# Kernel tuning notes

Hardware: AMD Instinct MI355X
Metric: run time of the kernel (lower is better)

Reference implementation:

```python
import jax, jax.numpy as jnp
import numpy as np

EPS = 1e-5

def layer_norm(x, w, b):
    # normalize over last two dims [N, H]
    mean = jnp.mean(x, axis=(-2, -1), keepdims=True)
    var = jnp.var(x, axis=(-2, -1), keepdims=True)
    return (x - mean) * jax.lax.rsqrt(var + EPS) * w + b

def lg_conv(x, edge_index, num_nodes):
    # LightGCN conv: symmetric-normalized neighbor sum (no self loops)
    src, dst = edge_index[0], edge_index[1]
    deg = jnp.zeros((num_nodes,), x.dtype).at[dst].add(1.0)
    dinv = jnp.where(deg > 0, jax.lax.rsqrt(jnp.maximum(deg, 1.0)), 0.0)
    norm = dinv[src] * dinv[dst]                      # [E]
    msgs = x[:, :, src, :] * norm[None, None, :, None]  # [B,P,E,H]
    return jnp.zeros_like(x).at[:, :, dst, :].add(msgs)

def setup_inputs() -> dict:
    key = jax.random.key(0)
    ks = jax.random.split(key, 4)
    B, P, N, H = 16, 12, 2048, 64
    E = 16384
    x = jax.random.normal(ks[0], (B, P, N, H), dtype=jnp.float32)
    edge_index = jax.random.randint(ks[1], (2, E), 0, N, dtype=jnp.int64)
    g_norm_w = jnp.ones((N, H), jnp.float32)
    g_norm_b = jnp.zeros((N, H), jnp.float32)
    t_norm_w = jnp.ones((N, H), jnp.float32)
    t_norm_b = jnp.zeros((N, H), jnp.float32)
    bound = 1.0 / np.sqrt(P)  # Conv2d default init range
    conv_w = jax.random.uniform(ks[2], (P, P), jnp.float32, -bound, bound)
    conv_b = jax.random.uniform(ks[3], (P,), jnp.float32, -bound, bound)
    return {"x": x, "edge_index": edge_index,
            "g_norm_w": g_norm_w, "g_norm_b": g_norm_b,
            "t_norm_w": t_norm_w, "t_norm_b": t_norm_b,
            "conv_w": conv_w, "conv_b": conv_b}

def reference(x, edge_index, g_norm_w, g_norm_b, t_norm_w, t_norm_b, conv_w, conv_b):
    N = x.shape[2]
    h = layer_norm(x, g_norm_w, g_norm_b)
    h = lg_conv(h, edge_index, N)
    h = layer_norm(h, t_norm_w, t_norm_b)
    # 1x1 Conv2d over channels = periods: [B,P,N,H] -> [B,Q,N,H]
    out = jnp.einsum('qp,bpnh->bqnh', conv_w, h) + conv_b[None, :, None, None]
    return out
```

## Files before the change

kernel.cpp:

```cpp
#include <hip/hip_runtime.h>

#define B_ 16
#define P_ 12
#define N_ 2048
#define H_ 64
#define E_ 16384
#define NH_ (N_*H_)
#define NG_ (B_*P_)

__global__ __launch_bounds__(256) void k_stats_x(const float* __restrict__ x,
                                                 float* __restrict__ partials ) {
    int g   = blockIdx.x >> 3;
    int seg = blockIdx.x & 7;
    const float4* xg = (const float4*)(x + (size_t)g * NH_);
    float s = 0.f, q = 0.f;
    int base = seg * 4096;
    #pragma unroll
    for (int i = 0; i < 16; ++i) {
        float4 v = xg[base + i*256 + threadIdx.x];
        s += v.x + v.y + v.z + v.w;
        q += v.x*v.x + v.y*v.y + v.z*v.z + v.w*v.w;
    }
    __shared__ float ls[4], lq[4];
    for (int off = 32; off; off >>= 1) { s += __shfl_down(s, off); q += __shfl_down(q, off); }
    int wid = threadIdx.x >> 6, lane = threadIdx.x & 63;
    if (!lane) { ls[wid] = s; lq[wid] = q; }
    __syncthreads();
    if (!threadIdx.x) {
        partials[blockIdx.x*2]   = ls[0]+ls[1]+ls[2]+ls[3];
        partials[blockIdx.x*2+1] = lq[0]+lq[1]+lq[2]+lq[3];
    }
}

__global__ __launch_bounds__(64) void k_finalize(const float* __restrict__ partials, int cnt,
                                                 float* __restrict__ mean, float* __restrict__ rstd) {
    int g = blockIdx.x, lane = threadIdx.x;
    float s = (lane < cnt) ? partials[(g*cnt+lane)*2]   : 0.f;
    float q = (lane < cnt) ? partials[(g*cnt+lane)*2+1] : 0.f;
    for (int off = 32; off; off >>= 1) { s += __shfl_down(s, off); q += __shfl_down(q, off); }
    if (!lane) {
        float m = s * (1.0f/NH_);
        float v = q * (1.0f/NH_) - m*m;
        mean[g] = m;
        rstd[g] = rsqrtf(v + 1e-5f);
    }
}

__global__ __launch_bounds__(1024) void k_build_csr(const int* __restrict__ ew,
                                                    int* __restrict__ rowPtr,
                                                    int* __restrict__ csrSrc,
                                                    float* __restrict__ csrW) {
    __shared__ int   sDeg[N_];
    __shared__ int   sA[N_];
    __shared__ int   sB[N_];
    __shared__ float sDinv[N_];
    __shared__ int   sFlag;
    int tid = threadIdx.x;
    if (!tid) sFlag = 1;
    for (int i = tid; i < N_; i += 1024) sDeg[i] = 0;
    __syncthreads();
    if (tid < 256) { if (ew[2*tid+1] != 0) atomicAnd(&sFlag, 0); }
    __syncthreads();
    int is64 = sFlag;
    for (int e = tid; e < E_; e += 1024) {
        int dst = is64 ? ew[2*(E_+e)] : ew[E_+e];
        atomicAdd(&sDeg[dst], 1);
    }
    __syncthreads();
    for (int i = tid; i < N_; i += 1024) {
        int d = sDeg[i];
        sDinv[i] = d > 0 ? rsqrtf((float)d) : 0.f;
        sA[i] = d;
    }
    __syncthreads();
    int* in = sA; int* out = sB;
    for (int st = 1; st < N_; st <<= 1) {
        for (int i = tid; i < N_; i += 1024) {
            int v = in[i];
            if (i >= st) v += in[i-st];
            out[i] = v;
        }
        __syncthreads();
        int* t = in; in = out; out = t;
    }
    for (int i = tid; i < N_; i += 1024) {
        int excl = in[i] - sDeg[i];
        rowPtr[i] = excl;
        out[i] = excl;
    }
    if (!tid) rowPtr[N_] = E_;
    __syncthreads();
    for (int e = tid; e < E_; e += 1024) {
        int src = is64 ? ew[2*e]       : ew[e];
        int dst = is64 ? ew[2*(E_+e)]  : ew[E_+e];
        int pos = atomicAdd(&out[dst], 1);
        csrSrc[pos] = src;
        csrW[pos] = sDinv[src] * sDinv[dst];
    }
}

__global__ __launch_bounds__(256) void k_gather(const float* __restrict__ x,
                                                const float* __restrict__ gw,
                                                const float* __restrict__ gb,
                                                const float* __restrict__ mean1,
                                                const float* __restrict__ rstd1,
                                                const int* __restrict__ rowPtr,
                                                const int* __restrict__ csrSrc,
                                                const float* __restrict__ csrW,
                                                float* __restrict__ h2,
                                                float* __restrict__ partials ) {
    int b     = blockIdx.x & 15;
    int chunk = blockIdx.x >> 4;
    int wid = threadIdx.x >> 6, lane = threadIdx.x & 63;
    __shared__ float s_rs[P_], s_mrs[P_];
    __shared__ float red[4][P_][2];
    if (threadIdx.x < P_) {
        float m = mean1[b*P_ + threadIdx.x], r = rstd1[b*P_ + threadIdx.x];
        s_rs[threadIdx.x] = r; s_mrs[threadIdx.x] = m*r;
    }
    __syncthreads();
    const float* xb = x + (size_t)b * P_ * NH_;
    float sp[P_], qp[P_];
    #pragma unroll
    for (int p = 0; p < P_; ++p) { sp[p] = 0.f; qp[p] = 0.f; }
    for (int i = 0; i < 8; ++i) {
        int n  = chunk*32 + wid*8 + i;
        int r0 = rowPtr[n], r1 = rowPtr[n+1];
        float acc[P_];
        #pragma unroll
        for (int p = 0; p < P_; ++p) acc[p] = 0.f;
        float An = 0.f, Bn = 0.f;
        for (int j = r0; j < r1; ++j) {
            int   src = csrSrc[j];
            float w   = csrW[j];
            int   ro  = src*H_ + lane;
            float t   = w * gw[ro];
            Bn += t;
            An += w * gb[ro];
            #pragma unroll
            for (int p = 0; p < P_; ++p)
                acc[p] += t * xb[(size_t)p*NH_ + ro];
        }
        size_t ob = (size_t)b*P_*NH_ + (size_t)n*H_ + lane;
        #pragma unroll
        for (int p = 0; p < P_; ++p) {
            float val = s_rs[p]*acc[p] - s_mrs[p]*Bn + An;
            h2[ob + (size_t)p*NH_] = val;
            sp[p] += val; qp[p] += val*val;
        }
    }
    #pragma unroll
    for (int p = 0; p < P_; ++p) {
        float s = sp[p], q = qp[p];
        for (int off = 32; off; off >>= 1) { s += __shfl_down(s, off); q += __shfl_down(q, off); }
        if (!lane) { red[wid][p][0] = s; red[wid][p][1] = q; }
    }
    __syncthreads();
    if (threadIdx.x < P_*2) {
        int p = threadIdx.x >> 1, c = threadIdx.x & 1;
        float v = red[0][p][c] + red[1][p][c] + red[2][p][c] + red[3][p][c];
        partials[(((b*P_ + p) << 6) + chunk)*2 + c] = v;
    }
}

__global__ __launch_bounds__(256) void k_mix(float* __restrict__ h2,
                                             const float* __restrict__ tw,
                                             const float* __restrict__ tb,
                                             const float* __restrict__ cw,
                                             const float* __restrict__ cb,
                                             const float* __restrict__ mean2,
                                             const float* __restrict__ rstd2) {
    __shared__ float scw[P_*P_], scb[P_], sm[P_], sr[P_], srow[P_];
    int b     = blockIdx.x >> 7;
    int chunk = blockIdx.x & 127;
    int tid   = threadIdx.x;
    if (tid < P_*P_) scw[tid] = cw[tid];
    if (tid < P_) {
        scb[tid] = cb[tid];
        sm[tid]  = mean2[b*P_ + tid];
        sr[tid]  = rstd2[b*P_ + tid];
    }
    __syncthreads();
    if (tid < P_) {
        float rs = 0.f;
        #pragma unroll
        for (int p = 0; p < P_; ++p) rs += scw[tid*P_ + p];
        srow[tid] = rs;
    }
    __syncthreads();
    int elem4 = chunk*256 + tid;
    size_t base = (size_t)b * P_ * NH_;
    float4 v[P_];
    #pragma unroll
    for (int p = 0; p < P_; ++p) {
        float4 t = *(const float4*)(h2 + base + (size_t)p*NH_ + (size_t)elem4*4);
        float m = sm[p], r = sr[p];
        v[p].x = (t.x-m)*r; v[p].y = (t.y-m)*r; v[p].z = (t.z-m)*r; v[p].w = (t.w-m)*r;
    }
    float4 tw4 = *(const float4*)(tw + (size_t)elem4*4);
    float4 tb4 = *(const float4*)(tb + (size_t)elem4*4);
    #pragma unroll
    for (int q = 0; q < P_; ++q) {
        float4 a = {0.f,0.f,0.f,0.f};
        #pragma unroll
        for (int p = 0; p < P_; ++p) {
            float c = scw[q*P_ + p];
            a.x += c*v[p].x; a.y += c*v[p].y; a.z += c*v[p].z; a.w += c*v[p].w;
        }
        float rb = srow[q], cbq = scb[q];
        float4 o;
        o.x = tw4.x*a.x + tb4.x*rb + cbq;
        o.y = tw4.y*a.y + tb4.y*rb + cbq;
        o.z = tw4.z*a.z + tb4.z*rb + cbq;
        o.w = tw4.w*a.w + tb4.w*rb + cbq;
        *(float4*)(h2 + base + (size_t)q*NH_ + (size_t)elem4*4) = o;
    }
}

extern "C" void kernel_launch(void* const* d_in, const int* in_sizes, int n_in,
                              void* d_out, int out_size, void* d_ws, size_t ws_size,
                              hipStream_t stream) {
    const float* x  = (const float*)d_in[0];
    const int*   ew = (const int*)d_in[1];
    const float* gw = (const float*)d_in[2];
    const float* gb = (const float*)d_in[3];
    const float* tw = (const float*)d_in[4];
    const float* tb = (const float*)d_in[5];
    const float* cw = (const float*)d_in[6];
    const float* cb = (const float*)d_in[7];
    float* out = (float*)d_out;
    float* wf  = (float*)d_ws;

    float* mean1  = wf + 0;
    float* rstd1  = wf + 192;
    float* mean2  = wf + 384;
    float* rstd2  = wf + 576;
    float* pA     = wf + 768;
    float* pC     = wf + 3840;
    int*   rowPtr = (int*)(wf + 28416);
    int*   csrSrc = (int*)(wf + 30468);
    float* csrW   = wf + 46852;

    k_stats_x<<<NG_*8, 256, 0, stream>>>(x, pA);
    k_finalize<<<NG_, 64, 0, stream>>>(pA, 8, mean1, rstd1);
    k_build_csr<<<1, 1024, 0, stream>>>(ew, rowPtr, csrSrc, csrW);
    k_gather<<<B_*64, 256, 0, stream>>>(x, gw, gb, mean1, rstd1,
                                        rowPtr, csrSrc, csrW, out, pC);
    k_finalize<<<NG_, 64, 0, stream>>>(pC, 64, mean2, rstd2);
    k_mix<<<B_*128, 256, 0, stream>>>(out, tw, tb, cw, cb, mean2, rstd2);
}
```

Baseline: 367.7 us.

## Fuse input stats with CSR build, double gather grid, prefetch edges

The separate x-statistics kernel, its finalize pass and the single-block CSR build are merged into one launch. The first 192 blocks compute each group's mean and rstd directly, and one extra block builds the CSR, so the serial CSR build overlaps with the stats pass and two launches go away. The gather kernel now handles 16 nodes per block instead of 32, doubling the grid, and it prefetches the next edge's source index and weight to shorten the dependent load chain. Second-pass partials grow to 128 per group, and finalize now loops to handle more than 64 entries.

```diff
diff --git a/kernel.cpp b/kernel.cpp
--- a/kernel.cpp
+++ b/kernel.cpp
@@ -8,45 +8,10 @@
 #define NH_ (N_*H_)
 #define NG_ (B_*P_)
 
-__global__ __launch_bounds__(256) void k_stats_x(const float* __restrict__ x,
-                                                 float* __restrict__ partials ) {
-    int g   = blockIdx.x >> 3;
-    int seg = blockIdx.x & 7;
-    const float4* xg = (const float4*)(x + (size_t)g * NH_);
-    float s = 0.f, q = 0.f;
-    int base = seg * 4096;
-    #pragma unroll
-    for (int i = 0; i < 16; ++i) {
-        float4 v = xg[base + i*256 + threadIdx.x];
-        s += v.x + v.y + v.z + v.w;
-        q += v.x*v.x + v.y*v.y + v.z*v.z + v.w*v.w;
-    }
-    __shared__ float ls[4], lq[4];
-    for (int off = 32; off; off >>= 1) { s += __shfl_down(s, off); q += __shfl_down(q, off); }
-    int wid = threadIdx.x >> 6, lane = threadIdx.x & 63;
-    if (!lane) { ls[wid] = s; lq[wid] = q; }
-    __syncthreads();
-    if (!threadIdx.x) {
-        partials[blockIdx.x*2]   = ls[0]+ls[1]+ls[2]+ls[3];
-        partials[blockIdx.x*2+1] = lq[0]+lq[1]+lq[2]+lq[3];
-    }
-}
-
-__global__ __launch_bounds__(64) void k_finalize(const float* __restrict__ partials, int cnt,
-                                                 float* __restrict__ mean, float* __restrict__ rstd) {
-    int g = blockIdx.x, lane = threadIdx.x;
-    float s = (lane < cnt) ? partials[(g*cnt+lane)*2]   : 0.f;
-    float q = (lane < cnt) ? partials[(g*cnt+lane)*2+1] : 0.f;
-    for (int off = 32; off; off >>= 1) { s += __shfl_down(s, off); q += __shfl_down(q, off); }
-    if (!lane) {
-        float m = s * (1.0f/NH_);
-        float v = q * (1.0f/NH_) - m*m;
-        mean[g] = m;
-        rstd[g] = rsqrtf(v + 1e-5f);
-    }
-}
-
-__global__ __launch_bounds__(1024) void k_build_csr(const int* __restrict__ ew,
+__global__ __launch_bounds__(1024) void k_stats_csr(const float* __restrict__ x,
+                                                    const int* __restrict__ ew,
+                                                    float* __restrict__ mean1,
+                                                    float* __restrict__ rstd1,
                                                     int* __restrict__ rowPtr,
                                                     int* __restrict__ csrSrc,
                                                     float* __restrict__ csrW) {
@@ -55,7 +20,33 @@
     __shared__ int   sB[N_];
     __shared__ float sDinv[N_];
     __shared__ int   sFlag;
+    __shared__ float ls[16], lq[16];
     int tid = threadIdx.x;
+    if (blockIdx.x < NG_) {
+        int g = blockIdx.x;
+        const float4* xg = (const float4*)(x + (size_t)g * NH_);
+        float s = 0.f, q = 0.f;
+        #pragma unroll 8
+        for (int i = 0; i < 32; ++i) {
+            float4 v = xg[i*1024 + tid];
+            s += v.x + v.y + v.z + v.w;
+            q += v.x*v.x + v.y*v.y + v.z*v.z + v.w*v.w;
+        }
+        for (int off = 32; off; off >>= 1) { s += __shfl_down(s, off); q += __shfl_down(q, off); }
+        int wid = tid >> 6, lane = tid & 63;
+        if (!lane) { ls[wid] = s; lq[wid] = q; }
+        __syncthreads();
+        if (!tid) {
+            float S = 0.f, Q = 0.f;
+            #pragma unroll
+            for (int i = 0; i < 16; ++i) { S += ls[i]; Q += lq[i]; }
+            float m = S * (1.0f/NH_);
+            float v = Q * (1.0f/NH_) - m*m;
+            mean1[g] = m;
+            rstd1[g] = rsqrtf(v + 1e-5f);
+        }
+        return;
+    }
     if (!tid) sFlag = 1;
     for (int i = tid; i < N_; i += 1024) sDeg[i] = 0;
     __syncthreads();
@@ -96,6 +87,23 @@
         int pos = atomicAdd(&out[dst], 1);
         csrSrc[pos] = src;
         csrW[pos] = sDinv[src] * sDinv[dst];
+    }
+}
+
+__global__ __launch_bounds__(64) void k_finalize(const float* __restrict__ partials, int cnt,
+                                                 float* __restrict__ mean, float* __restrict__ rstd) {
+    int g = blockIdx.x, lane = threadIdx.x;
+    float s = 0.f, q = 0.f;
+    for (int i = lane; i < cnt; i += 64) {
+        s += partials[(g*cnt+i)*2];
+        q += partials[(g*cnt+i)*2+1];
+    }
+    for (int off = 32; off; off >>= 1) { s += __shfl_down(s, off); q += __shfl_down(q, off); }
+    if (!lane) {
+        float m = s * (1.0f/NH_);
+        float v = q * (1.0f/NH_) - m*m;
+        mean[g] = m;
+        rstd[g] = rsqrtf(v + 1e-5f);
     }
 }
 
@@ -123,23 +131,31 @@
     float sp[P_], qp[P_];
     #pragma unroll
     for (int p = 0; p < P_; ++p) { sp[p] = 0.f; qp[p] = 0.f; }
-    for (int i = 0; i < 8; ++i) {
-        int n  = chunk*32 + wid*8 + i;
+    #pragma unroll
+    for (int i = 0; i < 4; ++i) {
+        int n  = chunk*16 + wid*4 + i;
         int r0 = rowPtr[n], r1 = rowPtr[n+1];
         float acc[P_];
         #pragma unroll
         for (int p = 0; p < P_; ++p) acc[p] = 0.f;
         float An = 0.f, Bn = 0.f;
-        for (int j = r0; j < r1; ++j) {
-            int   src = csrSrc[j];
-            float w   = csrW[j];
-            int   ro  = src*H_ + lane;
-            float t   = w * gw[ro];
-            Bn += t;
-            An += w * gb[ro];
-            #pragma unroll
-            for (int p = 0; p < P_; ++p)
-                acc[p] += t * xb[(size_t)p*NH_ + ro];
+        if (r0 < r1) {
+            int   src = csrSrc[r0];
+            float w   = csrW[r0];
+            for (int j = r0; j < r1; ++j) {
+                int   ro  = src*H_ + lane;
+                float gwv = gw[ro];
+                float gbv = gb[ro];
+                int   nsrc = 0; float nw = 0.f;
+                if (j+1 < r1) { nsrc = csrSrc[j+1]; nw = csrW[j+1]; }
+                float t = w * gwv;
+                Bn += t;
+                An += w * gbv;
+                #pragma unroll
+                for (int p = 0; p < P_; ++p)
+                    acc[p] += t * xb[(size_t)p*NH_ + ro];
+                src = nsrc; w = nw;
+            }
         }
         size_t ob = (size_t)b*P_*NH_ + (size_t)n*H_ + lane;
         #pragma unroll
@@ -159,7 +175,7 @@
     if (threadIdx.x < P_*2) {
         int p = threadIdx.x >> 1, c = threadIdx.x & 1;
         float v = red[0][p][c] + red[1][p][c] + red[2][p][c] + red[3][p][c];
-        partials[(((b*P_ + p) << 6) + chunk)*2 + c] = v;
+        partials[(((b*P_ + p) << 7) + chunk)*2 + c] = v;
     }
 }
 
@@ -235,17 +251,14 @@
     float* rstd1  = wf + 192;
     float* mean2  = wf + 384;
     float* rstd2  = wf + 576;
-    float* pA     = wf + 768;
-    float* pC     = wf + 3840;
-    int*   rowPtr = (int*)(wf + 28416);
-    int*   csrSrc = (int*)(wf + 30468);
-    float* csrW   = wf + 46852;
-
-    k_stats_x<<<NG_*8, 256, 0, stream>>>(x, pA);
-    k_finalize<<<NG_, 64, 0, stream>>>(pA, 8, mean1, rstd1);
-    k_build_csr<<<1, 1024, 0, stream>>>(ew, rowPtr, csrSrc, csrW);
-    k_gather<<<B_*64, 256, 0, stream>>>(x, gw, gb, mean1, rstd1,
-                                        rowPtr, csrSrc, csrW, out, pC);
-    k_finalize<<<NG_, 64, 0, stream>>>(pC, 64, mean2, rstd2);
+    float* pC     = wf + 768;
+    int*   rowPtr = (int*)(wf + 49920);
+    int*   csrSrc = (int*)(wf + 51972);
+    float* csrW   = wf + 68356;
+
+    k_stats_csr<<<NG_ + 1, 1024, 0, stream>>>(x, ew, mean1, rstd1, rowPtr, csrSrc, csrW);
+    k_gather<<<B_*128, 256, 0, stream>>>(x, gw, gb, mean1, rstd1,
+                                         rowPtr, csrSrc, csrW, out, pC);
+    k_finalize<<<NG_, 64, 0, stream>>>(pC, 128, mean2, rstd2);
     k_mix<<<B_*128, 256, 0, stream>>>(out, tw, tb, cw, cb, mean2, rstd2);
 }
```

New measurement: 357.4 us. -2.8%, faster.
